# Kernel optimization log

Hardware: AMD Instinct MI355X
Metric: run time of the kernel (lower is better)

The kernel has to match this reference:

```python
import jax, jax.numpy as jnp
import numpy as np

B, T, H = 2, 1024, 4096
HK, HV, DK, DV = 8, 32, 64, 64
VPK = HV // HK            # value heads per key head = 4
KEY_DIM = HK * DK         # 512
VAL_DIM = HV * DV         # 2048
CONV_DIM = 2 * KEY_DIM + VAL_DIM  # 3072
KSZ = 4
EPS = 1e-5
L2_EPS = 1e-6


def _l2norm(x):
    return x * jax.lax.rsqrt(jnp.sum(x * x, axis=-1, keepdims=True) + L2_EPS)


def setup_inputs() -> dict:
    key = jax.random.key(0)
    ks = jax.random.split(key, 8)
    s = 0.02
    return {
        "hidden_states": jax.random.normal(ks[0], (B, T, H), jnp.float32),
        "W_qkvz": jax.random.normal(ks[1], (H, 2 * KEY_DIM + 2 * VAL_DIM), jnp.float32) * s,
        "W_ba": jax.random.normal(ks[2], (H, 2 * HV), jnp.float32) * s,
        "conv_w": jax.random.normal(ks[3], (CONV_DIM, KSZ), jnp.float32) * 0.1,
        "dt_bias": jnp.ones((HV,), jnp.float32),
        "A_log": jnp.log(jax.random.uniform(ks[4], (HV,), jnp.float32, 1.0, 16.0)),
        "norm_w": jnp.ones((DV,), jnp.float32),
        "W_out": jax.random.normal(ks[5], (VAL_DIM, H), jnp.float32) * s,
    }


def _forward(hidden_states, W_qkvz, W_ba, conv_w, dt_bias, A_log, norm_w, W_out):
    # --- projections ---
    qkvz = hidden_states @ W_qkvz                       # [B,T,5120]
    ba = hidden_states @ W_ba                           # [B,T,64]
    # fix_query_key_value_ordering: per key head [q(Dk), k(Dk), v(vpk*Dv), z(vpk*Dv)]
    qkvz = qkvz.reshape(B, T, HK, 2 * DK + 2 * VPK * DV)
    q = qkvz[..., :DK]                                  # [B,T,HK,DK]
    k = qkvz[..., DK:2 * DK]
    v = qkvz[..., 2 * DK:2 * DK + VPK * DV].reshape(B, T, HV, DV)
    z = qkvz[..., 2 * DK + VPK * DV:].reshape(B, T, HV, DV)
    ba = ba.reshape(B, T, HK, 2 * VPK)
    b = ba[..., :VPK].reshape(B, T, HV)
    a = ba[..., VPK:].reshape(B, T, HV)

    # --- causal depthwise conv over concatenated qkv, then silu ---
    mixed = jnp.concatenate(
        [q.reshape(B, T, KEY_DIM), k.reshape(B, T, KEY_DIM), v.reshape(B, T, VAL_DIM)], axis=-1)
    padded = jnp.pad(mixed, ((0, 0), (KSZ - 1, 0), (0, 0)))
    conv = sum(padded[:, j:j + T, :] * conv_w[:, j] for j in range(KSZ))
    conv = jax.nn.silu(conv)
    q = conv[..., :KEY_DIM].reshape(B, T, HK, DK)
    k = conv[..., KEY_DIM:2 * KEY_DIM].reshape(B, T, HK, DK)
    v = conv[..., 2 * KEY_DIM:].reshape(B, T, HV, DV)

    # --- fused GDN gating: g = -exp(A_log)*softplus(a+dt_bias), beta = sigmoid(b) ---
    g = -jnp.exp(A_log) * jax.nn.softplus(a + dt_bias)  # [B,T,HV]
    beta = jax.nn.sigmoid(b)                            # [B,T,HV]

    # --- q/k l2 norm + scale, broadcast key heads to value heads ---
    q = _l2norm(q) * (DK ** -0.5)
    k = _l2norm(k)
    q = jnp.repeat(q, VPK, axis=2)                      # [B,T,HV,DK]
    k = jnp.repeat(k, VPK, axis=2)

    # --- gated delta-rule recurrence over time ---
    def step(S, inp):
        qt, kt, vt, gt, bt = inp                        # qt/kt [B,HV,DK], vt [B,HV,DV]
        S = S * jnp.exp(gt)[..., None, None]            # decay
        pred = jnp.einsum('bhk,bhkv->bhv', kt, S)
        delta = (vt - pred) * bt[..., None]
        S = S + jnp.einsum('bhk,bhv->bhkv', kt, delta)
        o = jnp.einsum('bhk,bhkv->bhv', qt, S)
        return S, o

    xs = (q.transpose(1, 0, 2, 3), k.transpose(1, 0, 2, 3), v.transpose(1, 0, 2, 3),
          g.transpose(1, 0, 2), beta.transpose(1, 0, 2))
    S0 = jnp.zeros((B, HV, DK, DV), q.dtype)
    _, o = jax.lax.scan(step, S0, xs)                   # [T,B,HV,DV]
    o = o.transpose(1, 0, 2, 3)                         # [B,T,HV,DV]

    # --- gated RMSNorm (norm before gate) + out projection ---
    o_n = o * jax.lax.rsqrt(jnp.mean(o * o, axis=-1, keepdims=True) + EPS) * norm_w
    o_n = o_n * jax.nn.silu(z)
    return o_n.reshape(B, T, VAL_DIM) @ W_out           # [B,T,H]


def reference(hidden_states, W_qkvz, W_ba, conv_w, dt_bias, A_log, norm_w, W_out):
    return _forward(hidden_states, W_qkvz, W_ba, conv_w, dt_bias, A_log, norm_w, W_out)
```

## Files before the change

### kernel.cpp

```cpp
#include <hip/hip_runtime.h>
#include <hip/hip_bf16.h>
#include <cstdint>
#include <cstddef>


typedef __attribute__((ext_vector_type(8))) short short8;
typedef __attribute__((ext_vector_type(4))) float f32x4;

__device__ __forceinline__ short f2bf(float f) {
  union { float f; unsigned u; } x; x.f = f;
  unsigned r = x.u + 0x7fffu + ((x.u >> 16) & 1u);
  return (short)(r >> 16);
}

__device__ __forceinline__ void gl_lds16(const short* g, short* l) {
  __builtin_amdgcn_global_load_lds(
      (const __attribute__((address_space(1))) void*)g,
      (__attribute__((address_space(3))) void*)l, 16, 0, 0);
}

__global__ __launch_bounds__(256) void prep_kernel(const float* __restrict__ hidden,
                                                   const float* __restrict__ Wq,
                                                   const float* __restrict__ Wba,
                                                   const float* __restrict__ Wo,
                                                   short* __restrict__ A_bf,
                                                   short* __restrict__ Wt1,
                                                   short* __restrict__ Wt2) {
  __shared__ float tile[32][33];
  const int bid = blockIdx.x;
  const int t = threadIdx.x;
  if (bid < 8192) {
    int i = bid * 256 + t;
    float4 v = ((const float4*)hidden)[i];
    ushort4 r;
    r.x = (unsigned short)f2bf(v.x);
    r.y = (unsigned short)f2bf(v.y);
    r.z = (unsigned short)f2bf(v.z);
    r.w = (unsigned short)f2bf(v.w);
    ((ushort4*)A_bf)[i] = r;
    return;
  }
  int r = t >> 5;
  int c = t & 31;
  if (bid < 8192 + 20992) {
    int b2 = bid - 8192;
    int n0 = (b2 % 164) * 32;
    int k0 = (b2 / 164) * 32;
#pragma unroll
    for (int i = 0; i < 4; ++i) {
      int kl = r + i * 8;
      int n = n0 + c;
      float v = 0.f;
      if (n < 5120) v = Wq[(size_t)(k0 + kl) * 5120 + n];
      else if (n < 5184) v = Wba[(size_t)(k0 + kl) * 64 + (n - 5120)];
      tile[kl][c] = v;
    }
    __syncthreads();
#pragma unroll
    for (int i = 0; i < 4; ++i) {
      int nl = r + i * 8;
      Wt1[(size_t)(n0 + nl) * 4096 + k0 + c] = f2bf(tile[c][nl]);
    }
    return;
  }
  int b3 = bid - 29184;
  int n0 = (b3 % 128) * 32;
  int k0 = (b3 / 128) * 32;
#pragma unroll
  for (int i = 0; i < 4; ++i) {
    int kl = r + i * 8;
    tile[kl][c] = Wo[(size_t)(k0 + kl) * 4096 + n0 + c];
  }
  __syncthreads();
#pragma unroll
  for (int i = 0; i < 4; ++i) {
    int nl = r + i * 8;
    Wt2[(size_t)(n0 + nl) * 2048 + k0 + c] = f2bf(tile[c][nl]);
  }
}

template <bool GUARD_N>
__global__ __launch_bounds__(256) void gemm128p(const short* __restrict__ A,
                                                const short* __restrict__ Bt,
                                                float* __restrict__ C,
                                                int N, int K, int MT) {
  __shared__ __align__(16) short As[3 * 4096];
  __shared__ __align__(16) short Bs[3 * 4096];
  const int tid = threadIdx.x;
  const int w = tid >> 6, lane = tid & 63;
  const int wm = w >> 1, wn = w & 1;

  const int nwg = gridDim.x;
  const int bid = blockIdx.x;
  const int swz = (bid & 7) * (nwg >> 3) + (bid >> 3);
  const int m0 = (swz % MT) * 128;
  const int n0 = (swz / MT) * 128;

  const int p0 = w * 64 + lane;
  const int rp0 = p0 >> 3, q0 = p0 & 7;
  const int mm0 = q0 ^ (rp0 & 7);
  const int srow = rp0 * 2 + (mm0 >> 2);
  const int scol = (mm0 & 3) << 3;
  const short* Ag = A + (size_t)(m0 + srow) * K + scol;
  const short* Bg = Bt + (size_t)(n0 + srow) * K + scol;
  const size_t rstep = (size_t)64 * K;

  const int fr = lane & 15;
  const int s = lane >> 4;
  int aoff[4], boff[4];
#pragma unroll
  for (int i = 0; i < 4; ++i) {
    int row = wm * 64 + i * 16 + fr;
    int rp = row >> 1;
    int q = (((row & 1) << 2) | s) ^ (rp & 7);
    aoff[i] = (rp * 8 + q) * 8;
  }
#pragma unroll
  for (int j = 0; j < 4; ++j) {
    int row = wn * 64 + j * 16 + fr;
    int rp = row >> 1;
    int q = (((row & 1) << 2) | s) ^ (rp & 7);
    boff[j] = (rp * 8 + q) * 8;
  }

  f32x4 acc[4][4];
#pragma unroll
  for (int i = 0; i < 4; ++i)
#pragma unroll
    for (int j = 0; j < 4; ++j) acc[i][j] = (f32x4){0.f, 0.f, 0.f, 0.f};

  const int NKT = K >> 5;

#define STAGE_A(kt, bb)                                                \
  { const short* g = Ag + (size_t)(kt) * 32;                           \
    gl_lds16(g,         &As[(bb) * 4096 + w * 512]);                   \
    gl_lds16(g + rstep, &As[(bb) * 4096 + 2048 + w * 512]); }
#define STAGE_B(kt, bb)                                                \
  { const short* g = Bg + (size_t)(kt) * 32;                           \
    gl_lds16(g,         &Bs[(bb) * 4096 + w * 512]);                   \
    gl_lds16(g + rstep, &Bs[(bb) * 4096 + 2048 + w * 512]); }

  STAGE_A(0, 0); STAGE_B(0, 0);
  STAGE_A(1, 1); STAGE_B(1, 1);
  asm volatile("s_waitcnt vmcnt(4)" ::: "memory");
  __builtin_amdgcn_s_barrier();
  __builtin_amdgcn_sched_barrier(0);

  int bi = 0;
  for (int kt = 0; kt < NKT; ++kt) {
    int bi2 = bi - 1; if (bi2 < 0) bi2 = 2;
    const short* Ab = &As[bi * 4096];
    const short* Bb = &Bs[bi * 4096];
    short8 af[2], bf[4];
#pragma unroll
    for (int i = 0; i < 2; ++i) af[i] = *(const short8*)&Ab[aoff[i]];
#pragma unroll
    for (int j = 0; j < 4; ++j) bf[j] = *(const short8*)&Bb[boff[j]];
    if (kt + 2 < NKT) STAGE_A(kt + 2, bi2);
    __builtin_amdgcn_s_barrier();
    asm volatile("s_waitcnt lgkmcnt(0)" ::: "memory");
    __builtin_amdgcn_sched_barrier(0);
    __builtin_amdgcn_s_setprio(1);
#pragma unroll
    for (int i = 0; i < 2; ++i)
#pragma unroll
      for (int j = 0; j < 4; ++j)
        acc[i][j] = __builtin_amdgcn_mfma_f32_16x16x32_bf16(af[i], bf[j], acc[i][j], 0, 0, 0);
    __builtin_amdgcn_s_setprio(0);
    __builtin_amdgcn_sched_barrier(0);
#pragma unroll
    for (int i = 0; i < 2; ++i) af[i] = *(const short8*)&Ab[aoff[i + 2]];
    if (kt + 2 < NKT) STAGE_B(kt + 2, bi2);
    if (kt < NKT - 2) { asm volatile("s_waitcnt vmcnt(4)" ::: "memory"); }
    else              { asm volatile("s_waitcnt vmcnt(0)" ::: "memory"); }
    __builtin_amdgcn_s_barrier();
    asm volatile("s_waitcnt lgkmcnt(0)" ::: "memory");
    __builtin_amdgcn_sched_barrier(0);
    __builtin_amdgcn_s_setprio(1);
#pragma unroll
    for (int i = 0; i < 2; ++i)
#pragma unroll
      for (int j = 0; j < 4; ++j)
        acc[i + 2][j] = __builtin_amdgcn_mfma_f32_16x16x32_bf16(af[i], bf[j], acc[i + 2][j], 0, 0, 0);
    __builtin_amdgcn_s_setprio(0);
    __builtin_amdgcn_sched_barrier(0);
    __builtin_amdgcn_s_barrier();
    ++bi; if (bi == 3) bi = 0;
  }
#undef STAGE_A
#undef STAGE_B

  const int rbase = (lane >> 4) << 2;
#pragma unroll
  for (int i = 0; i < 4; ++i) {
#pragma unroll
    for (int j = 0; j < 4; ++j) {
      int col = n0 + wn * 64 + j * 16 + fr;
      if (GUARD_N && col >= N) continue;
      int row = m0 + wm * 64 + i * 16 + rbase;
#pragma unroll
      for (int r = 0; r < 4; ++r)
        C[(size_t)(row + r) * N + col] = acc[i][j][r];
    }
  }
}

__global__ __launch_bounds__(256) void conv_kernel(const float* __restrict__ qkvz,
                                                   const float* __restrict__ conv_w,
                                                   const float* __restrict__ dt_bias,
                                                   const float* __restrict__ A_log,
                                                   float* __restrict__ mix,
                                                   float* __restrict__ gb,
                                                   float* __restrict__ beta) {
  __shared__ float sq[1024];
  __shared__ float scale[16];
  int bt = blockIdx.x;
  int t = bt & 1023;
  int tid = threadIdx.x;
#pragma unroll
  for (int it = 0; it < 3; ++it) {
    int c0 = (tid + it * 256) * 4;
    int col;
    if (c0 < 512) {
      col = (c0 >> 6) * 640 + (c0 & 63);
    } else if (c0 < 1024) {
      int c2 = c0 - 512;
      col = (c2 >> 6) * 640 + 64 + (c2 & 63);
    } else {
      int c3 = c0 - 1024;
      int hv = c3 >> 6;
      col = (hv >> 2) * 640 + 128 + (hv & 3) * 64 + (c3 & 63);
    }
    float cwa[4][4];
#pragma unroll
    for (int e = 0; e < 4; ++e) {
      float4 w4 = *(const float4*)(conv_w + (size_t)(c0 + e) * 4);
      cwa[e][0] = w4.x; cwa[e][1] = w4.y; cwa[e][2] = w4.z; cwa[e][3] = w4.w;
    }
    float4 acc = {0.f, 0.f, 0.f, 0.f};
#pragma unroll
    for (int j = 0; j < 4; ++j) {
      if (t - 3 + j >= 0) {
        float4 qv = *(const float4*)(qkvz + (size_t)(bt - 3 + j) * 5184 + col);
        acc.x += qv.x * cwa[0][j];
        acc.y += qv.y * cwa[1][j];
        acc.z += qv.z * cwa[2][j];
        acc.w += qv.w * cwa[3][j];
      }
    }
    float4 sv;
    sv.x = acc.x / (1.f + __expf(-acc.x));
    sv.y = acc.y / (1.f + __expf(-acc.y));
    sv.z = acc.z / (1.f + __expf(-acc.z));
    sv.w = acc.w / (1.f + __expf(-acc.w));
    if (c0 < 1024)
      *(float4*)&sq[c0] = sv;
    else
      *(float4*)(mix + (size_t)bt * 3072 + c0) = sv;
  }
  if (tid < 32) {
    int hv2 = tid;
    int hk2 = hv2 >> 2, vp = hv2 & 3;
    const float* row = qkvz + (size_t)bt * 5184 + 5120 + hk2 * 8;
    float bv = row[vp];
    float av = row[4 + vp];
    float x = av + dt_bias[hv2];
    float sp = (x > 20.f) ? x : log1pf(expf(x));
    gb[(size_t)bt * 32 + hv2] = -expf(A_log[hv2]) * sp;
    beta[(size_t)bt * 32 + hv2] = 1.f / (1.f + expf(-bv));
  }
  __syncthreads();
  int g = tid >> 4, l = tid & 15;
  float p = 0.f;
#pragma unroll
  for (int i = 0; i < 4; ++i) {
    float v = sq[g * 64 + l * 4 + i];
    p += v * v;
  }
  p += __shfl_xor(p, 1);
  p += __shfl_xor(p, 2);
  p += __shfl_xor(p, 4);
  p += __shfl_xor(p, 8);
  if (l == 0) scale[g] = rsqrtf(p + 1e-6f);
  __syncthreads();
  {
    int c0 = tid * 4;
    float s = scale[c0 >> 6] * ((c0 < 512) ? 0.125f : 1.f);
    float4 v = *(const float4*)&sq[c0];
    v.x *= s; v.y *= s; v.z *= s; v.w *= s;
    *(float4*)(mix + (size_t)bt * 3072 + c0) = v;
  }
}

__global__ __launch_bounds__(256) void precompute_kernel(
    const float* __restrict__ mix, const float* __restrict__ gbuf,
    const float* __restrict__ betab, float* __restrict__ Wbuf,
    float* __restrict__ Pbuf, float* __restrict__ Rbuf, float* __restrict__ cbuf) {
  __shared__ float Kt[64][68];
  __shared__ float Vb[64][68];
  __shared__ float AM[64][68];
  __shared__ float Mm[64][68];
  __shared__ float Tb[16][17];
  __shared__ float cs[64], bb[64];

  const int u = blockIdx.x;
  const int chunk = u & 15, hv = (u >> 4) & 31, b = u >> 9;
  const int hk = hv >> 2;
  const int t0g = b * 1024 + chunk * 64;
  const int tid = threadIdx.x;
  const int tr = tid >> 2, q4 = tid & 3;
  const int r4 = tid >> 4, c4 = tid & 15;

  {
    const float* mrow = mix + (size_t)(t0g + tr) * 3072;
#pragma unroll
    for (int e = 0; e < 4; ++e) {
      int c0 = q4 * 16 + e * 4;
      float4 kv = *(const float4*)(mrow + 512 + hk * 64 + c0);
      Kt[c0 + 0][tr] = kv.x; Kt[c0 + 1][tr] = kv.y;
      Kt[c0 + 2][tr] = kv.z; Kt[c0 + 3][tr] = kv.w;
      *(float4*)&Vb[tr][c0] = *(const float4*)(mrow + 1024 + hv * 64 + c0);
    }
  }
  if (tid < 64) {
    cs[tid] = gbuf[(size_t)(t0g + tid) * 32 + hv];
    bb[tid] = betab[(size_t)(t0g + tid) * 32 + hv];
  }
  __syncthreads();
  for (int off = 1; off < 64; off <<= 1) {
    float v = 0.f;
    if (tid < 64 && tid >= off) v = cs[tid - off];
    __syncthreads();
    if (tid < 64) cs[tid] += v;
    __syncthreads();
  }
  if (tid < 64) cbuf[(size_t)u * 64 + tid] = cs[tid];

  {
    float acc[4][4];
#pragma unroll
    for (int i = 0; i < 4; ++i)
#pragma unroll
      for (int j = 0; j < 4; ++j) acc[i][j] = 0.f;
    for (int d = 0; d < 64; ++d) {
      float4 a4 = *(const float4*)&Kt[d][r4 * 4];
      float4 b4 = *(const float4*)&Kt[d][c4 * 4];
      float av[4] = {a4.x, a4.y, a4.z, a4.w};
      float bv[4] = {b4.x, b4.y, b4.z, b4.w};
#pragma unroll
      for (int i = 0; i < 4; ++i)
#pragma unroll
        for (int j = 0; j < 4; ++j) acc[i][j] += av[i] * bv[j];
    }
    float4 cc = *(const float4*)&cs[c4 * 4];
    float ccv[4] = {cc.x, cc.y, cc.z, cc.w};
#pragma unroll
    for (int i = 0; i < 4; ++i) {
      int row = r4 * 4 + i;
      float bt_ = bb[row], ct_ = cs[row];
      float ov[4];
#pragma unroll
      for (int j = 0; j < 4; ++j) {
        int sc = c4 * 4 + j;
        ov[j] = (sc < row) ? bt_ * acc[i][j] * __expf(ct_ - ccv[j]) : 0.f;
      }
      float4 o4 = {ov[0], ov[1], ov[2], ov[3]};
      *(float4*)&AM[row][c4 * 4] = o4;
    }
  }
  __syncthreads();

  for (int i = tid; i < 64 * 68; i += 256) (&Mm[0][0])[i] = 0.f;
  __syncthreads();
  if (tid < 64) {
    int blk = tid >> 4, j = tid & 15, base = blk * 16;
    Mm[base][base + j] = (j == 0) ? 1.f : 0.f;
    for (int r = 1; r < 16; ++r) {
      float sum = 0.f;
      for (int s = 0; s < r; ++s) sum += AM[base + r][base + s] * Mm[base + s][base + j];
      Mm[base + r][base + j] = ((r == j) ? 1.f : 0.f) - sum;
    }
  }
  __syncthreads();
  for (int d = 1; d < 4; ++d) {
    for (int j = 0; j + d < 4; ++j) {
      int i = j + d;
      int r = tid >> 4, c = tid & 15;
      float tsum = 0.f;
      for (int kb = j; kb < i; ++kb)
        for (int uu = 0; uu < 16; ++uu)
          tsum += AM[i * 16 + r][kb * 16 + uu] * Mm[kb * 16 + uu][j * 16 + c];
      Tb[r][c] = tsum;
      __syncthreads();
      float msum = 0.f;
      for (int uu = 0; uu < 16; ++uu)
        msum += Mm[i * 16 + r][i * 16 + uu] * Tb[uu][c];
      __syncthreads();
      Mm[i * 16 + r][j * 16 + c] = -msum;
      __syncthreads();
    }
  }

  {
    const float* mrow = mix + (size_t)(t0g + tr) * 3072 + hk * 64;
#pragma unroll
    for (int e = 0; e < 4; ++e) {
      int c0 = q4 * 16 + e * 4;
      float4 qv = *(const float4*)(mrow + c0);
      AM[c0 + 0][tr] = qv.x; AM[c0 + 1][tr] = qv.y;
      AM[c0 + 2][tr] = qv.z; AM[c0 + 3][tr] = qv.w;
    }
  }
  __syncthreads();

  {
    float acc[4][4];
#pragma unroll
    for (int i = 0; i < 4; ++i)
#pragma unroll
      for (int j = 0; j < 4; ++j) acc[i][j] = 0.f;
    for (int d = 0; d < 64; ++d) {
      float4 a4 = *(const float4*)&AM[d][r4 * 4];
      float4 b4 = *(const float4*)&Kt[d][c4 * 4];
      float av[4] = {a4.x, a4.y, a4.z, a4.w};
      float bv[4] = {b4.x, b4.y, b4.z, b4.w};
#pragma unroll
      for (int i = 0; i < 4; ++i)
#pragma unroll
        for (int j = 0; j < 4; ++j) acc[i][j] += av[i] * bv[j];
    }
    float4 cc = *(const float4*)&cs[c4 * 4];
    float ccv[4] = {cc.x, cc.y, cc.z, cc.w};
#pragma unroll
    for (int i = 0; i < 4; ++i) {
      int row = r4 * 4 + i;
      float ct_ = cs[row];
      float pv[4];
#pragma unroll
      for (int j = 0; j < 4; ++j) {
        int sc = c4 * 4 + j;
        pv[j] = (sc <= row) ? acc[i][j] * __expf(ct_ - ccv[j]) : 0.f;
      }
      float4 p4 = {pv[0], pv[1], pv[2], pv[3]};
      *(float4*)&Pbuf[(size_t)u * 4096 + row * 64 + c4 * 4] = p4;
    }
  }
  __syncthreads();

  {
    float vals[16];
#pragma unroll
    for (int j = 0; j < 16; ++j) vals[j] = Kt[q4 * 16 + j][tr];
    float sc = bb[tr] * __expf(cs[tr]);
    __syncthreads();
#pragma unroll
    for (int j = 0; j < 16; ++j) Kt[tr][q4 * 16 + j] = vals[j] * sc;
  }
  __syncthreads();

  {
    float aw[4][4], ar[4][4];
#pragma unroll
    for (int i = 0; i < 4; ++i)
#pragma unroll
      for (int j = 0; j < 4; ++j) { aw[i][j] = 0.f; ar[i][j] = 0.f; }
    for (int s0 = 0; s0 < 64; s0 += 4) {
      float4 am[4];
#pragma unroll
      for (int i = 0; i < 4; ++i) am[i] = *(const float4*)&Mm[r4 * 4 + i][s0];
      float4 bq = *(const float4*)&bb[s0];
      float bbv[4] = {bq.x, bq.y, bq.z, bq.w};
      float kv[4][4], vv[4][4];
#pragma unroll
      for (int uu = 0; uu < 4; ++uu) {
        float4 k4 = *(const float4*)&Kt[s0 + uu][c4 * 4];
        float4 v4 = *(const float4*)&Vb[s0 + uu][c4 * 4];
        kv[uu][0] = k4.x; kv[uu][1] = k4.y; kv[uu][2] = k4.z; kv[uu][3] = k4.w;
        vv[uu][0] = v4.x; vv[uu][1] = v4.y; vv[uu][2] = v4.z; vv[uu][3] = v4.w;
      }
#pragma unroll
      for (int i = 0; i < 4; ++i) {
        float amv[4] = {am[i].x, am[i].y, am[i].z, am[i].w};
#pragma unroll
        for (int uu = 0; uu < 4; ++uu) {
          float mw = amv[uu];
          float mr = mw * bbv[uu];
#pragma unroll
          for (int j = 0; j < 4; ++j) {
            aw[i][j] += mw * kv[uu][j];
            ar[i][j] += mr * vv[uu][j];
          }
        }
      }
    }
#pragma unroll
    for (int i = 0; i < 4; ++i) {
      int row = r4 * 4 + i;
      float4 w4 = {aw[i][0], aw[i][1], aw[i][2], aw[i][3]};
      float4 rr = {ar[i][0], ar[i][1], ar[i][2], ar[i][3]};
      *(float4*)&Wbuf[(size_t)u * 4096 + row * 64 + c4 * 4] = w4;
      *(float4*)&Rbuf[(size_t)u * 4096 + row * 64 + c4 * 4] = rr;
    }
  }
}

__global__ __launch_bounds__(256) void precompute2_kernel(
    const float* __restrict__ mix, const float* __restrict__ cbuf,
    float* __restrict__ Wbuf, float* __restrict__ Pbuf, float* __restrict__ Rbuf,
    float* __restrict__ Hbuf) {
  __shared__ float At[64][132];
  __shared__ float Bsm[64][188];

  const int u = blockIdx.x;
  const int chunk = u & 15, hv = (u >> 4) & 31, b = u >> 9;
  const int hk = hv >> 2;
  const int t0g = b * 1024 + chunk * 64;
  const int tid = threadIdx.x;
  const int tr = tid >> 2, q4 = tid & 3;

  const float c63 = cbuf[(size_t)u * 64 + 63];
  const float csr = cbuf[(size_t)u * 64 + tr];
  const float sKv = __expf(c63 - csr);

  {
    const float* Pr = Pbuf + (size_t)u * 4096 + tr * 64;
#pragma unroll
    for (int e = 0; e < 4; ++e) {
      int k0 = q4 * 16 + e * 4;
      float4 p4 = *(const float4*)(Pr + k0);
      At[k0 + 0][tr] = p4.x; At[k0 + 1][tr] = p4.y;
      At[k0 + 2][tr] = p4.z; At[k0 + 3][tr] = p4.w;
    }
    const float* Kr = mix + (size_t)(t0g + tr) * 3072 + 512 + hk * 64;
#pragma unroll
    for (int e = 0; e < 4; ++e) {
      int n = q4 * 16 + e * 4;
      float4 k4 = *(const float4*)(Kr + n);
      float4 o4 = {k4.x * sKv, k4.y * sKv, k4.z * sKv, k4.w * sKv};
      *(float4*)&At[tr][64 + n] = o4;
    }
  }
  {
    const float* Wr = Wbuf + (size_t)u * 4096 + tr * 64;
    const float* Rr = Rbuf + (size_t)u * 4096 + tr * 64;
#pragma unroll
    for (int e = 0; e < 4; ++e) {
      int n = q4 * 16 + e * 4;
      int cp = n + ((n >> 3) << 2);
      *(float4*)&Bsm[tr][cp] = *(const float4*)(Wr + n);
      *(float4*)&Bsm[tr][cp + 96] = *(const float4*)(Rr + n);
    }
  }
  __syncthreads();

  const int m0 = (tid >> 4) << 3;
  const int n0 = (tid & 15) << 3;
  const int cb = n0 + ((n0 >> 3) << 2);
  float acc[8][8];
#pragma unroll
  for (int i = 0; i < 8; ++i)
#pragma unroll
    for (int j = 0; j < 8; ++j) acc[i][j] = 0.f;

  for (int k = 0; k < 64; ++k) {
    float4 a0 = *(const float4*)&At[k][m0];
    float4 a1 = *(const float4*)&At[k][m0 + 4];
    float4 b0 = *(const float4*)&Bsm[k][cb];
    float4 b1 = *(const float4*)&Bsm[k][cb + 4];
    float am[8] = {a0.x, a0.y, a0.z, a0.w, a1.x, a1.y, a1.z, a1.w};
    float bn[8] = {b0.x, b0.y, b0.z, b0.w, b1.x, b1.y, b1.z, b1.w};
#pragma unroll
    for (int i = 0; i < 8; ++i)
#pragma unroll
      for (int j = 0; j < 8; ++j) acc[i][j] += am[i] * bn[j];
  }

  if (m0 < 64) {
    if (n0 < 64) {
#pragma unroll
      for (int i = 0; i < 8; ++i) {
        int t = m0 + i;
        float ee = __expf(cbuf[(size_t)u * 64 + t]);
        const float* Qr = mix + (size_t)(t0g + t) * 3072 + hk * 64 + n0;
        float4 q0 = *(const float4*)(Qr);
        float4 q1 = *(const float4*)(Qr + 4);
        float4 g0 = {q0.x * ee - acc[i][0], q0.y * ee - acc[i][1],
                     q0.z * ee - acc[i][2], q0.w * ee - acc[i][3]};
        float4 g1 = {q1.x * ee - acc[i][4], q1.y * ee - acc[i][5],
                     q1.z * ee - acc[i][6], q1.w * ee - acc[i][7]};
        float* dst = Wbuf + (size_t)u * 4096 + t * 64 + n0;
        *(float4*)dst = g0; *(float4*)(dst + 4) = g1;
      }
    } else {
#pragma unroll
      for (int i = 0; i < 8; ++i) {
        float* dst = Rbuf + (size_t)u * 4096 + (m0 + i) * 64 + (n0 - 64);
        float4 r0 = {acc[i][0], acc[i][1], acc[i][2], acc[i][3]};
        float4 r1 = {acc[i][4], acc[i][5], acc[i][6], acc[i][7]};
        *(float4*)dst = r0; *(float4*)(dst + 4) = r1;
      }
    }
  } else {
    if (n0 < 64) {
#pragma unroll
      for (int i = 0; i < 8; ++i) {
        float* dst = Hbuf + (size_t)u * 4096 + (m0 - 64 + i) * 64 + n0;
        float4 h0 = {acc[i][0], acc[i][1], acc[i][2], acc[i][3]};
        float4 h1 = {acc[i][4], acc[i][5], acc[i][6], acc[i][7]};
        *(float4*)dst = h0; *(float4*)(dst + 4) = h1;
      }
    } else {
#pragma unroll
      for (int i = 0; i < 8; ++i) {
        float* dst = Pbuf + (size_t)u * 4096 + (m0 - 64 + i) * 64 + (n0 - 64);
        float4 k0v = {acc[i][0], acc[i][1], acc[i][2], acc[i][3]};
        float4 k1v = {acc[i][4], acc[i][5], acc[i][6], acc[i][7]};
        *(float4*)dst = k0v; *(float4*)(dst + 4) = k1v;
      }
    }
  }
}

__global__ __launch_bounds__(512) void chunk_scan_kernel(
    const float* __restrict__ Gbuf, const float* __restrict__ Hbuf,
    const float* __restrict__ ORbuf, const float* __restrict__ KRbuf,
    const float* __restrict__ cbuf, float* __restrict__ o) {
  __shared__ float Gs[64][68], Hs[64][68];
  __shared__ float St[16][68];

  const int bid = blockIdx.x;
  const int vs = bid & 3, hv = (bid >> 2) & 31, b = bid >> 7;
  const int bh = b * 32 + hv;
  const int ubase = bh * 16;
  const int tid = threadIdx.x;
  const int tr = tid >> 3, q8 = tid & 7;
  const int c0 = q8 * 2, c1 = q8 * 2 + 1;

  for (int i = tid; i < 16 * 68; i += 512) (&St[0][0])[i] = 0.f;

  float4 GN[2], HN[2];
  float2 ORn, KRn;
  float e63n = 0.f;

#define ISSUE(ch)                                                               \
  {                                                                             \
    size_t uu = (size_t)(ubase + (ch));                                         \
    _Pragma("unroll") for (int i = 0; i < 2; ++i) {                             \
      GN[i] = ((const float4*)(Gbuf + uu * 4096))[tid + 512 * i];               \
      HN[i] = ((const float4*)(Hbuf + uu * 4096))[tid + 512 * i];               \
    }                                                                           \
    ORn = *(const float2*)(ORbuf + uu * 4096 + tr * 64 + vs * 16 + q8 * 2);     \
    KRn = *(const float2*)(KRbuf + uu * 4096 + tr * 64 + vs * 16 + q8 * 2);     \
    e63n = cbuf[uu * 64 + 63];                                                  \
  }

#define COMMIT()                                                                \
  {                                                                             \
    _Pragma("unroll") for (int i = 0; i < 2; ++i) {                             \
      int flat = (tid + 512 * i) * 4;                                           \
      int rr = flat >> 6, cc = flat & 63;                                       \
      *(float4*)&Gs[rr][cc] = GN[i];                                            \
      *(float4*)&Hs[rr][cc] = HN[i];                                            \
    }                                                                           \
  }

  ISSUE(0);
  COMMIT();
  float2 ORv = ORn, KRv = KRn;
  float e63 = __expf(e63n);
  __syncthreads();

  for (int c = 0; c < 16; ++c) {
    if (c < 15) ISSUE(c + 1);
    float op0 = ORv.x, op1 = ORv.y, sn0 = KRv.x, sn1 = KRv.y;
    float sold0 = St[c0][tr], sold1 = St[c1][tr];
#pragma unroll
    for (int i = 0; i < 16; ++i) {
      float4 g4 = *(const float4*)&Gs[tr][i * 4];
      float4 h4 = *(const float4*)&Hs[tr][i * 4];
      float4 sa = *(const float4*)&St[c0][i * 4];
      float4 sb = *(const float4*)&St[c1][i * 4];
      op0 += g4.x * sa.x + g4.y * sa.y + g4.z * sa.z + g4.w * sa.w;
      op1 += g4.x * sb.x + g4.y * sb.y + g4.z * sb.z + g4.w * sb.w;
      sn0 -= h4.x * sa.x + h4.y * sa.y + h4.z * sa.z + h4.w * sa.w;
      sn1 -= h4.x * sb.x + h4.y * sb.y + h4.z * sb.z + h4.w * sb.w;
    }
    *(float2*)&o[((size_t)(bh * 4 + vs) * 1024 + c * 64 + tr) * 16 + q8 * 2] =
        (float2){op0, op1};
    float snew0 = sold0 * e63 + sn0;
    float snew1 = sold1 * e63 + sn1;
    __syncthreads();
    St[c0][tr] = snew0;
    St[c1][tr] = snew1;
    if (c < 15) {
      COMMIT();
      ORv = ORn; KRv = KRn; e63 = __expf(e63n);
    }
    __syncthreads();
  }
#undef ISSUE
#undef COMMIT
}

__global__ __launch_bounds__(256) void rms_gate_kernel(const float* __restrict__ o,
                                                       const float* __restrict__ qkvz,
                                                       const float* __restrict__ norm_w,
                                                       short* __restrict__ on) {
  int bid = blockIdx.x;
  int bh = bid >> 6;
  int tg = bid & 63;
  int b = bh >> 5, hv = bh & 31;
  int r = threadIdx.x >> 4;
  int d4 = threadIdx.x & 15;
  int t = tg * 16 + r;
  int d = d4 * 4;
  int bt = b * 1024 + t;
  int hk = hv >> 2, vp = hv & 3;
  float4 x4 = *(const float4*)&o[((size_t)(bh * 4 + (d >> 4)) * 1024 + t) * 16 + (d & 15)];
  float ss = x4.x * x4.x + x4.y * x4.y + x4.z * x4.z + x4.w * x4.w;
  ss += __shfl_xor(ss, 1);
  ss += __shfl_xor(ss, 2);
  ss += __shfl_xor(ss, 4);
  ss += __shfl_xor(ss, 8);
  float sc = rsqrtf(ss * (1.f / 64.f) + 1e-5f);
  float4 z4 = *(const float4*)&qkvz[(size_t)bt * 5184 + hk * 640 + 384 + vp * 64 + d];
  float4 w4 = *(const float4*)&norm_w[d];
  ushort4 out4;
  float v0 = x4.x * sc * w4.x * (z4.x / (1.f + __expf(-z4.x)));
  float v1 = x4.y * sc * w4.y * (z4.y / (1.f + __expf(-z4.y)));
  float v2 = x4.z * sc * w4.z * (z4.z / (1.f + __expf(-z4.z)));
  float v3 = x4.w * sc * w4.w * (z4.w / (1.f + __expf(-z4.w)));
  out4.x = (unsigned short)f2bf(v0);
  out4.y = (unsigned short)f2bf(v1);
  out4.z = (unsigned short)f2bf(v2);
  out4.w = (unsigned short)f2bf(v3);
  *(ushort4*)&on[((size_t)bt * 32 + hv) * 64 + d] = out4;
}

extern "C" void kernel_launch(void* const* d_in, const int* in_sizes, int n_in,
                              void* d_out, int out_size, void* d_ws, size_t ws_size,
                              hipStream_t stream) {
  const float* hidden = (const float*)d_in[0];
  const float* W_qkvz = (const float*)d_in[1];
  const float* W_ba = (const float*)d_in[2];
  const float* conv_w = (const float*)d_in[3];
  const float* dt_bias = (const float*)d_in[4];
  const float* A_log = (const float*)d_in[5];
  const float* norm_w = (const float*)d_in[6];
  const float* W_out = (const float*)d_in[7];
  float* out = (float*)d_out;

  char* ws = (char*)d_ws;
  short* A_bf = (short*)(ws + 0);
  float* Hbuf = (float*)(ws + 0);
  short* Wt1 = (short*)(ws + 16777216);
  short* Wt2 = (short*)(ws + 59768832);
  float* qkvz = (float*)(ws + 76546048);
  float* mix = (float*)(ws + 119013376);
  float* gbuf = (float*)(ws + 144179200);
  float* beta = (float*)(ws + 144441344);
  float* o = (float*)(ws + 144703488);
  short* on = (short*)(ws + 161480704);
  float* Wbuf = (float*)(ws + 169869312);
  float* Pbuf = (float*)(ws + 186646528);
  float* Rbuf = (float*)(ws + 203423744);
  float* cbuf = (float*)(ws + 220200960);

  prep_kernel<<<37376, 256, 0, stream>>>(hidden, W_qkvz, W_ba, W_out, A_bf, Wt1, Wt2);
  gemm128p<true><<<656, 256, 0, stream>>>(A_bf, Wt1, qkvz, 5184, 4096, 16);
  conv_kernel<<<2048, 256, 0, stream>>>(qkvz, conv_w, dt_bias, A_log, mix, gbuf, beta);
  precompute_kernel<<<1024, 256, 0, stream>>>(mix, gbuf, beta, Wbuf, Pbuf, Rbuf, cbuf);
  precompute2_kernel<<<1024, 256, 0, stream>>>(mix, cbuf, Wbuf, Pbuf, Rbuf, Hbuf);
  chunk_scan_kernel<<<256, 512, 0, stream>>>(Wbuf, Hbuf, Rbuf, Pbuf, cbuf, o);
  rms_gate_kernel<<<4096, 256, 0, stream>>>(o, qkvz, norm_w, on);
  gemm128p<false><<<512, 256, 0, stream>>>(on, Wt2, out, 4096, 2048, 16);
}
```

Measured before the change: 522.5 us.

## Use 256x256-tile 8-wave pipelined GEMM for the input projection

Adds a new bf16 MFMA GEMM kernel with 256x256 output tiles, 8 waves and a double-buffered LDS pipeline with interleaved global-to-LDS prefetch, barriers and priority hints. It replaces the 128x128 GEMM for the qkvz/ba projection, cutting the grid from 656 to 168 workgroups. The larger tiles are meant to raise operand reuse and lower global traffic. The cost is fewer workgroups than CUs (168 on a 256-CU part), heavy register use, and out-of-range B rows clamped to the last valid row (5247).

```diff
diff --git a/kernel.cpp b/kernel.cpp
--- a/kernel.cpp
+++ b/kernel.cpp
@@ -76,6 +76,140 @@
   for (int i = 0; i < 4; ++i) {
     int nl = r + i * 8;
     Wt2[(size_t)(n0 + nl) * 2048 + k0 + c] = f2bf(tile[c][nl]);
+  }
+}
+
+template <bool GUARD_N>
+__global__ __launch_bounds__(512) void gemm256p8(const short* __restrict__ A,
+                                                 const short* __restrict__ Bt,
+                                                 float* __restrict__ C,
+                                                 int N, int NROWS, int K, int MT) {
+  __shared__ __align__(16) short As[2 * 16384];
+  __shared__ __align__(16) short Bs[2 * 16384];
+  const int tid = threadIdx.x;
+  const int w = tid >> 6, lane = tid & 63;
+  const int wm = w >> 2, wn = w & 3;
+
+  const int nwg = gridDim.x;
+  const int bid = blockIdx.x;
+  const int swz = (bid & 7) * (nwg >> 3) + (bid >> 3);
+  const int m0 = (swz % MT) * 256;
+  const int n0 = (swz / MT) * 256;
+
+  const int srow = tid >> 3;
+  const int skl = (tid & 7) ^ (srow & 7);
+  const short* Ag = A + (size_t)(m0 + srow) * K + skl * 8;
+  const short* Bg[4];
+#pragma unroll
+  for (int hh = 0; hh < 2; ++hh)
+#pragma unroll
+    for (int rr = 0; rr < 2; ++rr) {
+      int row = n0 + hh * 128 + rr * 64 + srow;
+      if (row > NROWS - 1) row = NROWS - 1;
+      Bg[hh * 2 + rr] = Bt + (size_t)row * K + skl * 8;
+    }
+
+  const int fr = lane & 15;
+  const int s = lane >> 4;
+  const int sl0 = (s ^ (fr & 7)) * 8;
+  const int sl1 = sl0 ^ 32;
+  int arow[8], brow[4];
+#pragma unroll
+  for (int i = 0; i < 8; ++i) arow[i] = (wm * 128 + i * 16 + fr) * 64;
+#pragma unroll
+  for (int j = 0; j < 4; ++j) brow[j] = (wn * 64 + j * 16 + fr) * 64;
+
+  f32x4 acc[8][4];
+#pragma unroll
+  for (int i = 0; i < 8; ++i)
+#pragma unroll
+    for (int j = 0; j < 4; ++j) acc[i][j] = (f32x4){0.f, 0.f, 0.f, 0.f};
+
+  const int NKT = K >> 6;
+  const int nIt = NKT >> 1;
+  short8 af[4], bf[4];
+
+#define STAGE_A(kt, hh)                                                     \
+  { const short* g = Ag + (size_t)(kt) * 64 + (size_t)(hh) * 128 * K;       \
+    gl_lds16(g,                  &As[((kt)&1) * 16384 + (hh) * 8192 + tid * 8]);        \
+    gl_lds16(g + (size_t)64 * K, &As[((kt)&1) * 16384 + (hh) * 8192 + 4096 + tid * 8]); }
+#define STAGE_B(kt, hh)                                                     \
+  { gl_lds16(Bg[(hh)*2+0] + (size_t)(kt) * 64, &Bs[((kt)&1) * 16384 + (hh) * 8192 + tid * 8]);        \
+    gl_lds16(Bg[(hh)*2+1] + (size_t)(kt) * 64, &Bs[((kt)&1) * 16384 + (hh) * 8192 + 4096 + tid * 8]); }
+#define RD_B(buf, sl)                                                       \
+  { _Pragma("unroll") for (int j = 0; j < 4; ++j)                           \
+      bf[j] = *(const short8*)&Bs[(buf) * 16384 + brow[j] + (sl)]; }
+#define RD_A(buf, mq, sl)                                                   \
+  { _Pragma("unroll") for (int i = 0; i < 4; ++i)                           \
+      af[i] = *(const short8*)&As[(buf) * 16384 + arow[(mq) * 4 + i] + (sl)]; }
+#define DO_MFMA(mq)                                                         \
+  { _Pragma("unroll") for (int i = 0; i < 4; ++i)                           \
+    _Pragma("unroll") for (int j = 0; j < 4; ++j)                           \
+      acc[(mq) * 4 + i][j] = __builtin_amdgcn_mfma_f32_16x16x32_bf16(       \
+          af[i], bf[j], acc[(mq) * 4 + i][j], 0, 0, 0); }
+#define BARS_PRE()                                                          \
+  __builtin_amdgcn_s_barrier();                                             \
+  asm volatile("s_waitcnt lgkmcnt(0)" ::: "memory");                        \
+  __builtin_amdgcn_sched_barrier(0);                                        \
+  __builtin_amdgcn_s_setprio(1);
+#define BARS_POST()                                                         \
+  __builtin_amdgcn_s_setprio(0);                                            \
+  __builtin_amdgcn_sched_barrier(0);                                        \
+  __builtin_amdgcn_s_barrier();
+
+  STAGE_A(0, 0); STAGE_B(0, 0); STAGE_A(0, 1); STAGE_B(0, 1);
+  STAGE_A(1, 0); STAGE_B(1, 0); STAGE_B(1, 1);
+  asm volatile("s_waitcnt vmcnt(6)" ::: "memory");
+  __builtin_amdgcn_s_barrier();
+  __builtin_amdgcn_sched_barrier(0);
+
+  for (int it = 0; it < nIt; ++it) {
+    const int T = it * 2;
+    const bool pf2 = (T + 2 < NKT);
+    const bool pf3 = (T + 3 < NKT);
+    RD_B(0, sl0); RD_A(0, 0, sl0);
+    STAGE_A(T + 1, 1);
+    BARS_PRE(); DO_MFMA(0); BARS_POST();
+    RD_A(0, 1, sl0);
+    BARS_PRE(); DO_MFMA(1); BARS_POST();
+    RD_B(0, sl1); RD_A(0, 0, sl1);
+    BARS_PRE(); DO_MFMA(0); BARS_POST();
+    RD_A(0, 1, sl1);
+    if (pf2) { STAGE_A(T + 2, 0); STAGE_B(T + 2, 0); }
+    asm volatile("s_waitcnt vmcnt(4)" ::: "memory");
+    BARS_PRE(); DO_MFMA(1); BARS_POST();
+    RD_B(1, sl0); RD_A(1, 0, sl0);
+    if (pf2) { STAGE_A(T + 2, 1); STAGE_B(T + 2, 1); }
+    BARS_PRE(); DO_MFMA(0); BARS_POST();
+    RD_A(1, 1, sl0);
+    BARS_PRE(); DO_MFMA(1); BARS_POST();
+    RD_B(1, sl1); RD_A(1, 0, sl1);
+    BARS_PRE(); DO_MFMA(0); BARS_POST();
+    RD_A(1, 1, sl1);
+    if (pf3) { STAGE_A(T + 3, 0); STAGE_B(T + 3, 0); STAGE_B(T + 3, 1); }
+    asm volatile("s_waitcnt vmcnt(6)" ::: "memory");
+    BARS_PRE(); DO_MFMA(1); BARS_POST();
+  }
+#undef STAGE_A
+#undef STAGE_B
+#undef RD_B
+#undef RD_A
+#undef DO_MFMA
+#undef BARS_PRE
+#undef BARS_POST
+
+  const int rbase = (lane >> 4) << 2;
+#pragma unroll
+  for (int i = 0; i < 8; ++i) {
+#pragma unroll
+    for (int j = 0; j < 4; ++j) {
+      int col = n0 + wn * 64 + j * 16 + fr;
+      if (GUARD_N && col >= N) continue;
+      int row = m0 + wm * 128 + i * 16 + rbase;
+#pragma unroll
+      for (int r = 0; r < 4; ++r)
+        C[(size_t)(row + r) * N + col] = acc[i][j][r];
+    }
   }
 }
 
@@ -767,7 +901,7 @@
   float* cbuf = (float*)(ws + 220200960);
 
   prep_kernel<<<37376, 256, 0, stream>>>(hidden, W_qkvz, W_ba, W_out, A_bf, Wt1, Wt2);
-  gemm128p<true><<<656, 256, 0, stream>>>(A_bf, Wt1, qkvz, 5184, 4096, 16);
+  gemm256p8<true><<<168, 512, 0, stream>>>(A_bf, Wt1, qkvz, 5184, 5248, 4096, 8);
   conv_kernel<<<2048, 256, 0, stream>>>(qkvz, conv_w, dt_bias, A_log, mix, gbuf, beta);
   precompute_kernel<<<1024, 256, 0, stream>>>(mix, gbuf, beta, Wbuf, Pbuf, Rbuf, cbuf);
   precompute2_kernel<<<1024, 256, 0, stream>>>(mix, cbuf, Wbuf, Pbuf, Rbuf, Hbuf);
```

Result: slower. 536.7 us (+2.7%).
